# Optimization experiments

Hardware: AMD Instinct MI355X
Metric: run time of the kernel (lower is better)

## Reference

```python
import jax, jax.numpy as jnp
import numpy as np

N_NODES, N_EDGES, N_GRAPHS = 100000, 1600000, 1000
DIN, DMID, DGLOB, DOUT = 128, 128, 64, 2


def setup_inputs() -> dict:
    key = jax.random.key(0)
    ks = jax.random.split(key, 12)
    x = jax.random.normal(ks[0], (N_NODES, DIN), dtype=jnp.float32)
    edge_index = jax.random.randint(ks[1], (2, N_EDGES), 0, N_NODES, dtype=jnp.int64 if jax.config.jax_enable_x64 else jnp.int32)
    u = jax.random.normal(ks[2], (N_GRAPHS, DGLOB), dtype=jnp.float32)
    batch = jnp.sort(jax.random.randint(ks[3], (N_NODES,), 0, N_GRAPHS))
    s = 1.0 / np.sqrt(DMID)
    W1 = jax.random.normal(ks[4], (DIN, DMID), dtype=jnp.float32) * s
    b1 = jnp.zeros((DMID,), dtype=jnp.float32)
    W2 = jax.random.normal(ks[5], (DMID, DMID), dtype=jnp.float32) * s
    b2 = jnp.zeros((DMID,), dtype=jnp.float32)
    Wh1 = jax.random.normal(ks[6], (DMID + DGLOB, DMID), dtype=jnp.float32) * s
    bh1 = jnp.zeros((DMID,), dtype=jnp.float32)
    Wh2 = jax.random.normal(ks[7], (DMID, DOUT), dtype=jnp.float32) * s
    bh2 = jnp.zeros((DOUT,), dtype=jnp.float32)
    return {"x": x, "edge_index": edge_index, "u": u, "batch": batch,
            "batch_size": N_GRAPHS, "W1": W1, "b1": b1, "W2": W2, "b2": b2,
            "Wh1": Wh1, "bh1": bh1, "Wh2": Wh2, "bh2": bh2}


def _gcn_conv(x, W, b, row, col, norm, n):
    # PyG GCNConv: linear transform then symmetric-normalized scatter-add
    h = x @ W                                    # [N, dmid]
    msg = norm[:, None] * h[row]                 # gather along source nodes
    out = jax.ops.segment_sum(msg, col, num_segments=n)  # scatter to dst
    return out + b


def reference(x, edge_index, u, batch, batch_size, W1, b1, W2, b2, Wh1, bh1, Wh2, bh2):
    n = x.shape[0]
    # add self-loops (GCNConv default, edge_weight=None -> all-ones weights)
    loop = jnp.arange(n, dtype=edge_index.dtype)
    row = jnp.concatenate([edge_index[0], loop])
    col = jnp.concatenate([edge_index[1], loop])
    deg = jax.ops.segment_sum(jnp.ones_like(col, dtype=x.dtype), col, num_segments=n)
    dinv = jnp.where(deg > 0, jax.lax.rsqrt(jnp.maximum(deg, 1e-12)), 0.0)
    norm = dinv[row] * dinv[col]                 # D^-1/2 A D^-1/2, shared by both layers

    h = jax.nn.relu(_gcn_conv(x, W1, b1, row, col, norm, n))
    h = jax.nn.relu(_gcn_conv(h, W2, b2, row, col, norm, n))

    # mean pool per graph
    sums = jax.ops.segment_sum(h, batch, num_segments=batch_size)
    cnt = jax.ops.segment_sum(jnp.ones((n,), dtype=h.dtype), batch, num_segments=batch_size)
    graph_emb = sums / jnp.maximum(cnt, 1.0)[:, None]

    hcat = jnp.concatenate([graph_emb, u], axis=-1)
    # head MLP (dropout in eval mode = identity)
    out = jax.nn.relu(hcat @ Wh1 + bh1) @ Wh2 + bh2
    return out
```

## Files before the change

kernel.cpp:

```cpp
#include <hip/hip_runtime.h>
#include <hip/hip_bf16.h>

#define NN 100000
#define NE 1600000
#define NG 1000
#define NBK 196
#define BSH 9
#define SLOT 10240
#define SLOTC 12288

typedef short short8 __attribute__((ext_vector_type(8)));
typedef float f32x4 __attribute__((ext_vector_type(4)));
typedef float f32x2 __attribute__((ext_vector_type(2)));

static inline int cdiv(int a, int b) { return (a + b - 1) / b; }

__device__ __forceinline__ unsigned short f2b(float f) {
    unsigned int u = __float_as_uint(f);
    u += 0x7fff + ((u >> 16) & 1);
    return (unsigned short)(u >> 16);
}
__device__ __forceinline__ unsigned int pack2(float lo, float hi) {
    return (unsigned int)f2b(lo) | ((unsigned int)f2b(hi) << 16);
}

template <int W>
__device__ __forceinline__ f32x2 f8_2f(unsigned int v) {
    return __builtin_amdgcn_cvt_pk_f32_fp8((int)v, W);
}
__device__ __forceinline__ unsigned int f2f8_lo(float a, float b, unsigned int old) {
    return (unsigned int)__builtin_amdgcn_cvt_pk_fp8_f32(a, b, (int)old, false);
}
__device__ __forceinline__ unsigned int f2f8_hi(float a, float b, unsigned int old) {
    return (unsigned int)__builtin_amdgcn_cvt_pk_fp8_f32(a, b, (int)old, true);
}
__device__ __forceinline__ unsigned char f2f8s(float a) {
    return (unsigned char)(__builtin_amdgcn_cvt_pk_fp8_f32(a, a, 0, false) & 0xFF);
}

__global__ __launch_bounds__(256) void k_prep(const float* __restrict__ W1,
                                              const float* __restrict__ W2,
                                              const float* __restrict__ b1,
                                              const float* __restrict__ b2,
                                              unsigned short* __restrict__ Wt1,
                                              unsigned char* __restrict__ Wt2p,
                                              float* __restrict__ b1p,
                                              float* __restrict__ b2p,
                                              int* __restrict__ gcur,
                                              const int* __restrict__ batch,
                                              int* __restrict__ gstart,
                                              unsigned char* __restrict__ Hs8) {
    int b = blockIdx.x, t = threadIdx.x;
    if (b < 128) {
        if (t < 128) {
            Wt1[b * 128 + t] = f2b(W1[t * 128 + b]);
        } else {
            int q = t - 128;
            int c = (q & 7) * 16 + (q >> 3);
            Wt2p[b * 128 + q] = f2f8s(W2[c * 128 + b]);
        }
    } else if (b == 128) {
        if (t < NBK) gcur[t] = t * SLOT;
        if (t < 128) {
            int c = (t & 7) * 16 + (t >> 3);
            b1p[t] = b1[c];
            b2p[t] = b2[c];
        }
        if (t >= 128 && t < 136) {
            uint4 z; z.x = 0u; z.y = 0u; z.z = 0u; z.w = 0u;
            ((uint4*)(Hs8 + (size_t)NN * 128))[t - 128] = z;
        }
    } else {
        int n = (b - 129) * 256 + t;
        if (n <= NN) {
            int cur = (n == NN) ? NG : batch[n];
            int prev = (n == 0) ? -1 : batch[n - 1];
            for (int g = prev + 1; g <= cur; g++) gstart[g] = n;
        }
    }
}

__global__ __launch_bounds__(256) void k_bin2(const int* __restrict__ row,
                                              const int* __restrict__ col,
                                              int* __restrict__ gcur,
                                              unsigned int* __restrict__ tmp) {
    __shared__ unsigned int ent[4000];
    __shared__ unsigned int srt[4000];
    __shared__ unsigned char bkt[4000];
    __shared__ unsigned char bky[4000];
    __shared__ int cnt[NBK];
    __shared__ int gbase[NBK];
    __shared__ int lbase[NBK];
    __shared__ int sh[256];
    int t = threadIdx.x;
    if (t < NBK) cnt[t] = 0;
    __syncthreads();
    const int q0 = blockIdx.x * 1000;
    const int4* col4 = (const int4*)col;
    const int4* row4 = (const int4*)row;
#pragma unroll
    for (int it = 0; it < 4; it++) {
        int idx = it * 256 + t;
        if (idx < 1000) {
            int4 c = col4[q0 + idx];
            int4 r = row4[q0 + idx];
            int d, b;
            d = c.x; b = d >> BSH; atomicAdd(&cnt[b], 1);
            ent[idx * 4 + 0] = ((unsigned int)(d & 511) << 17) | (unsigned int)r.x;
            bkt[idx * 4 + 0] = (unsigned char)b;
            d = c.y; b = d >> BSH; atomicAdd(&cnt[b], 1);
            ent[idx * 4 + 1] = ((unsigned int)(d & 511) << 17) | (unsigned int)r.y;
            bkt[idx * 4 + 1] = (unsigned char)b;
            d = c.z; b = d >> BSH; atomicAdd(&cnt[b], 1);
            ent[idx * 4 + 2] = ((unsigned int)(d & 511) << 17) | (unsigned int)r.z;
            bkt[idx * 4 + 2] = (unsigned char)b;
            d = c.w; b = d >> BSH; atomicAdd(&cnt[b], 1);
            ent[idx * 4 + 3] = ((unsigned int)(d & 511) << 17) | (unsigned int)r.w;
            bkt[idx * 4 + 3] = (unsigned char)b;
        }
    }
    __syncthreads();
    int v = (t < NBK) ? cnt[t] : 0;
    sh[t] = v;
    __syncthreads();
    for (int d = 1; d < 256; d <<= 1) {
        int u = (t >= d) ? sh[t - d] : 0;
        __syncthreads();
        sh[t] += u;
        __syncthreads();
    }
    if (t < NBK) {
        lbase[t] = sh[t] - v;
        gbase[t] = atomicAdd(&gcur[t], v);
        cnt[t] = sh[t] - v;
    }
    __syncthreads();
#pragma unroll
    for (int it = 0; it < 16; it++) {
        int i = it * 256 + t;
        if (i < 4000) {
            int b = bkt[i];
            int p = atomicAdd(&cnt[b], 1);
            srt[p] = ent[i];
            bky[p] = (unsigned char)b;
        }
    }
    __syncthreads();
#pragma unroll
    for (int it = 0; it < 16; it++) {
        int i = it * 256 + t;
        if (i < 4000) {
            int b = bky[i];
            tmp[gbase[b] + (i - lbase[b])] = srt[i];
        }
    }
}

__global__ __launch_bounds__(1024) void k_bucket(const unsigned int* __restrict__ tmp,
                                                 const int* __restrict__ gcur,
                                                 unsigned int* __restrict__ meta,
                                                 float* __restrict__ dinv,
                                                 int* __restrict__ csr_src) {
    __shared__ int cnt[512];
    __shared__ int loff[512];
    __shared__ int send[512];
    __shared__ int sh[256];
    int b = blockIdx.x, t = threadIdx.x;
    int j0 = b << BSH;
    int nd = min(512, NN - j0);
    int rb = b * SLOT;
    int rbc = b * SLOTC;
    int m = gcur[b] - rb;
    if (t < 512) cnt[t] = 0;
    __syncthreads();
    for (int i = t; i < m; i += 1024)
        atomicAdd(&cnt[tmp[rb + i] >> 17], 1);
    __syncthreads();
    int r0 = 0, r1 = 0, p0 = 0, ts = 0;
    if (t < 256) {
        r0 = cnt[2 * t]; r1 = cnt[2 * t + 1];
        p0 = (r0 + 7) & ~7;
        int p1 = (r1 + 7) & ~7;
        ts = p0 + p1;
        sh[t] = ts;
    }
    __syncthreads();
    for (int d = 1; d < 256; d <<= 1) {
        int u = (t >= d && t < 256) ? sh[t - d] : 0;
        __syncthreads();
        if (t < 256) sh[t] += u;
        __syncthreads();
    }
    if (t < 256) {
        int ex = sh[t] - ts;
        loff[2 * t] = ex;
        loff[2 * t + 1] = ex + p0;
    }
    __syncthreads();
    for (int j = t; j < nd; j += 1024) {
        int o = rbc + loff[j];
        int dg = cnt[j];
        int dgp = (dg + 7) & ~7;
        meta[j0 + j] = (unsigned int)o | ((unsigned int)dgp << 22);
        send[j] = o + dgp;
        dinv[j0 + j] = rsqrtf((float)(dg + 1));
        cnt[j] = o;
    }
    __syncthreads();
    for (int i = t; i < m; i += 1024) {
        unsigned int e = tmp[rb + i];
        int d = e >> 17;
        int s = (int)(e & 0x1FFFFu);
        int p = atomicAdd(&cnt[d], 1);
        csr_src[p] = s;
    }
    __syncthreads();
    for (int j = t; j < nd; j += 1024) {
        int pe = send[j];
        for (int p = cnt[j]; p < pe; p++) csr_src[p] = NN;
    }
}

__global__ __launch_bounds__(256) void k_gemm1(const float* __restrict__ X,
                                               const unsigned short* __restrict__ Wt,
                                               const float* __restrict__ dinv,
                                               unsigned char* __restrict__ Hs8) {
    __shared__ __align__(16) unsigned short Ws[128 * 128];
    int t = threadIdx.x;
#pragma unroll
    for (int i = 0; i < 8; i++) {
        int id = t + i * 256;
        int n = id >> 4, c = id & 15;
        *(short8*)((char*)Ws + n * 256 + ((c ^ (n & 15)) << 4)) =
            *(const short8*)(Wt + n * 128 + c * 8);
    }
    __syncthreads();

    int lane = t & 63, wid = t >> 6;
    int n16 = lane & 15, quad = lane >> 4;
    int row_base = blockIdx.x * 128 + wid * 32;

    short8 a[2][4];
#pragma unroll
    for (int rt = 0; rt < 2; rt++) {
        int r = row_base + rt * 16 + n16;
        if (r > NN - 1) r = NN - 1;
        const float* ap = X + (size_t)r * 128 + quad * 8;
#pragma unroll
        for (int ks = 0; ks < 4; ks++) {
            float4 v0 = *(const float4*)(ap + ks * 32);
            float4 v1 = *(const float4*)(ap + ks * 32 + 4);
            uint4 up;
            up.x = pack2(v0.x, v0.y); up.y = pack2(v0.z, v0.w);
            up.z = pack2(v1.x, v1.y); up.w = pack2(v1.z, v1.w);
            a[rt][ks] = *(short8*)&up;
        }
    }

    f32x4 acc[2][8];
#pragma unroll
    for (int rt = 0; rt < 2; rt++)
#pragma unroll
        for (int ct = 0; ct < 8; ct++)
            acc[rt][ct] = (f32x4){0.f, 0.f, 0.f, 0.f};

#pragma unroll
    for (int ks = 0; ks < 4; ks++) {
#pragma unroll
        for (int ct = 0; ct < 8; ct++) {
            short8 b = *(const short8*)((const char*)Ws +
                        (ct * 16 + n16) * 256 + ((((ks << 2) + quad) ^ n16) << 4));
            acc[0][ct] = __builtin_amdgcn_mfma_f32_16x16x32_bf16(a[0][ks], b, acc[0][ct], 0, 0, 0);
            acc[1][ct] = __builtin_amdgcn_mfma_f32_16x16x32_bf16(a[1][ks], b, acc[1][ct], 0, 0, 0);
        }
    }

#pragma unroll
    for (int rt = 0; rt < 2; rt++) {
#pragma unroll
        for (int reg = 0; reg < 4; reg++) {
            int row = row_base + rt * 16 + quad * 4 + reg;
            if (row < NN) {
                float di = dinv[row];
                unsigned int u0 = 0, u1 = 0;
                u0 = f2f8_lo(acc[rt][0][reg] * di, acc[rt][1][reg] * di, u0);
                u0 = f2f8_hi(acc[rt][2][reg] * di, acc[rt][3][reg] * di, u0);
                u1 = f2f8_lo(acc[rt][4][reg] * di, acc[rt][5][reg] * di, u1);
                u1 = f2f8_hi(acc[rt][6][reg] * di, acc[rt][7][reg] * di, u1);
                uint2 o; o.x = u0; o.y = u1;
                ((uint2*)(Hs8 + (size_t)row * 128))[n16] = o;
            }
        }
    }
}

__global__ __launch_bounds__(256) void k_gemm2(const unsigned char* __restrict__ A8,
                                               const unsigned char* __restrict__ Wt2p,
                                               const float* __restrict__ dinv,
                                               unsigned char* __restrict__ Hs8) {
    __shared__ __align__(16) unsigned char Ws[128 * 128];
    int t = threadIdx.x;
#pragma unroll
    for (int i = 0; i < 8; i++) {
        int id = t + i * 256;
        int n = id >> 4, c = id & 15;
        *(uint2*)(Ws + n * 128 + ((c ^ (n & 15)) << 3)) =
            *(const uint2*)(Wt2p + n * 128 + c * 8);
    }
    __syncthreads();

    int lane = t & 63, wid = t >> 6;
    int n16 = lane & 15, quad = lane >> 4;
    int row_base = blockIdx.x * 128 + wid * 32;

    uint2 a[2][4];
#pragma unroll
    for (int rt = 0; rt < 2; rt++) {
        int r = row_base + rt * 16 + n16;
        if (r > NN - 1) r = NN - 1;
        const unsigned char* ap = A8 + (size_t)r * 128 + quad * 8;
#pragma unroll
        for (int ks = 0; ks < 4; ks++)
            a[rt][ks] = *(const uint2*)(ap + ks * 32);
    }

    f32x4 acc[2][8];
#pragma unroll
    for (int rt = 0; rt < 2; rt++)
#pragma unroll
        for (int ct = 0; ct < 8; ct++)
            acc[rt][ct] = (f32x4){0.f, 0.f, 0.f, 0.f};

#pragma unroll
    for (int ks = 0; ks < 4; ks++) {
        long a0 = __builtin_bit_cast(long, a[0][ks]);
        long a1 = __builtin_bit_cast(long, a[1][ks]);
#pragma unroll
        for (int ct = 0; ct < 8; ct++) {
            uint2 bv = *(const uint2*)(Ws + (ct * 16 + n16) * 128 +
                                       ((((ks << 2) + quad) ^ n16) << 3));
            long bb = __builtin_bit_cast(long, bv);
            acc[0][ct] = __builtin_amdgcn_mfma_f32_16x16x32_fp8_fp8(a0, bb, acc[0][ct], 0, 0, 0);
            acc[1][ct] = __builtin_amdgcn_mfma_f32_16x16x32_fp8_fp8(a1, bb, acc[1][ct], 0, 0, 0);
        }
    }

#pragma unroll
    for (int rt = 0; rt < 2; rt++) {
#pragma unroll
        for (int reg = 0; reg < 4; reg++) {
            int row = row_base + rt * 16 + quad * 4 + reg;
            if (row < NN) {
                float di = dinv[row];
                unsigned int u0 = 0, u1 = 0;
                u0 = f2f8_lo(acc[rt][0][reg] * di, acc[rt][1][reg] * di, u0);
                u0 = f2f8_hi(acc[rt][2][reg] * di, acc[rt][3][reg] * di, u0);
                u1 = f2f8_lo(acc[rt][4][reg] * di, acc[rt][5][reg] * di, u1);
                u1 = f2f8_hi(acc[rt][6][reg] * di, acc[rt][7][reg] * di, u1);
                uint2 o; o.x = u0; o.y = u1;
                ((uint2*)(Hs8 + (size_t)row * 128))[n16] = o;
            }
        }
    }
}

__global__ __launch_bounds__(256) void k_agg(const unsigned char* __restrict__ Hb,
                                             const unsigned int* __restrict__ meta,
                                             const int* __restrict__ csr_src,
                                             const float* __restrict__ dinv,
                                             const float* __restrict__ biasp,
                                             unsigned char* __restrict__ outp) {
    int node = blockIdx.x * 16 + (threadIdx.x >> 4);
    int li = threadIdx.x & 15;
    unsigned lo8 = (unsigned)li * 8u;
    unsigned int md = meta[node];
    int base = (int)(md & 0x3FFFFFu);
    int degp = (int)(md >> 22);
    f32x2 A0 = {0.f, 0.f}, A1 = {0.f, 0.f}, A2 = {0.f, 0.f}, A3 = {0.f, 0.f};
#define LDH(idx) (*(const uint2*)(Hb + (unsigned)(idx) * 128u + lo8))
#define ACC8(V) { \
        A0 += f8_2f<0>((V).x); A1 += f8_2f<1>((V).x); \
        A2 += f8_2f<0>((V).y); A3 += f8_2f<1>((V).y); }
    uint2 v = LDH(node);
    const int4* ip = (const int4*)(csr_src + base);
    int4 i0 = ip[0], i1 = ip[1], i2 = ip[2], i3 = ip[3];
    ACC8(v)
    for (int e0 = 0; e0 < degp; e0 += 16) {
        uint2 w0 = LDH(i0.x), w1 = LDH(i0.y), w2 = LDH(i0.z), w3 = LDH(i0.w);
        uint2 w4 = LDH(i1.x), w5 = LDH(i1.y), w6 = LDH(i1.z), w7 = LDH(i1.w);
        uint2 w8 = {0, 0}, w9 = {0, 0}, wA = {0, 0}, wB = {0, 0};
        uint2 wC = {0, 0}, wD = {0, 0}, wE = {0, 0}, wF = {0, 0};
        if (e0 + 8 < degp) {
            w8 = LDH(i2.x); w9 = LDH(i2.y); wA = LDH(i2.z); wB = LDH(i2.w);
            wC = LDH(i3.x); wD = LDH(i3.y); wE = LDH(i3.z); wF = LDH(i3.w);
        }
        if (e0 + 16 < degp) {
            const int4* np = (const int4*)(csr_src + base + e0 + 16);
            i0 = np[0]; i1 = np[1]; i2 = np[2]; i3 = np[3];
        }
        ACC8(w0) ACC8(w1) ACC8(w2) ACC8(w3)
        ACC8(w4) ACC8(w5) ACC8(w6) ACC8(w7)
        ACC8(w8) ACC8(w9) ACC8(wA) ACC8(wB)
        ACC8(wC) ACC8(wD) ACC8(wE) ACC8(wF)
    }
#undef ACC8
#undef LDH
    float di = dinv[node];
    const float4* b4 = (const float4*)biasp;
    float4 bA = b4[li * 2], bB = b4[li * 2 + 1];
    float r0 = fmaxf(fmaf(di, A0[0], bA.x), 0.f);
    float r1 = fmaxf(fmaf(di, A0[1], bA.y), 0.f);
    float r2 = fmaxf(fmaf(di, A1[0], bA.z), 0.f);
    float r3 = fmaxf(fmaf(di, A1[1], bA.w), 0.f);
    float r4 = fmaxf(fmaf(di, A2[0], bB.x), 0.f);
    float r5 = fmaxf(fmaf(di, A2[1], bB.y), 0.f);
    float r6 = fmaxf(fmaf(di, A3[0], bB.z), 0.f);
    float r7 = fmaxf(fmaf(di, A3[1], bB.w), 0.f);
    unsigned int u0 = 0, u1 = 0;
    u0 = f2f8_lo(r0, r1, u0); u0 = f2f8_hi(r2, r3, u0);
    u1 = f2f8_lo(r4, r5, u1); u1 = f2f8_hi(r6, r7, u1);
    uint2 o; o.x = u0; o.y = u1;
    *(uint2*)(outp + (unsigned)node * 128u + lo8) = o;
}

__global__ __launch_bounds__(256) void k_poolhead(const unsigned char* __restrict__ A,
                                                  const int* __restrict__ gstart,
                                                  const float* __restrict__ u,
                                                  const float* __restrict__ Wh1,
                                                  const float* __restrict__ bh1,
                                                  const float* __restrict__ Wh2,
                                                  const float* __restrict__ bh2,
                                                  float* __restrict__ out) {
    int g = blockIdx.x, t = threadIdx.x;
    int start = gstart[g];
    int end = gstart[g + 1];

    int li = t & 7;
    int ri = t >> 3;
    float acc[16];
#pragma unroll
    for (int j = 0; j < 16; j++) acc[j] = 0.f;
    f32x2 p;
    for (int i = start + ri; i < end; i += 32) {
        uint4 v = ((const uint4*)A)[(size_t)i * 8 + li];
#define UP(VV, base) p = f8_2f<0>(VV); acc[base] += p.x; acc[base+1] += p.y; \
                     p = f8_2f<1>(VV); acc[base+2] += p.x; acc[base+3] += p.y;
        UP(v.x, 0) UP(v.y, 4) UP(v.z, 8) UP(v.w, 12)
#undef UP
    }
#pragma unroll
    for (int j = 0; j < 16; j++) {
        acc[j] += __shfl_xor(acc[j], 8);
        acc[j] += __shfl_xor(acc[j], 16);
        acc[j] += __shfl_xor(acc[j], 32);
    }
    __shared__ float part[4][128];
    __shared__ float hc[192];
    __shared__ float tt[128];
    int w = t >> 6;
    if ((t & 63) < 8) {
#pragma unroll
        for (int j = 0; j < 16; j++) part[w][li * 16 + j] = acc[j];
    }
    __syncthreads();
    float cntf = (float)max(end - start, 1);
    if (t < 128) {
        int q = (t & 15) * 8 + (t >> 4);
        hc[t] = (part[0][q] + part[1][q] + part[2][q] + part[3][q]) / cntf;
    } else if (t < 192) {
        hc[t] = u[g * 64 + (t - 128)];
    }
    __syncthreads();
    if (t < 128) {
        float a2 = bh1[t];
        for (int k = 0; k < 192; k++) a2 = fmaf(hc[k], Wh1[k * 128 + t], a2);
        tt[t] = fmaxf(a2, 0.f);
    }
    __syncthreads();
    if (t < 2) {
        float o = bh2[t];
        for (int c2 = 0; c2 < 128; c2++) o = fmaf(tt[c2], Wh2[c2 * 2 + t], o);
        out[g * 2 + t] = o;
    }
}

extern "C" void kernel_launch(void* const* d_in, const int* in_sizes, int n_in,
                              void* d_out, int out_size, void* d_ws, size_t ws_size,
                              hipStream_t stream) {
    const float* x   = (const float*)d_in[0];
    const int*   ei  = (const int*)d_in[1];
    const int*   row = ei;
    const int*   col = ei + NE;
    const float* u   = (const float*)d_in[2];
    const int*   batch = (const int*)d_in[3];
    const float* W1  = (const float*)d_in[5];
    const float* b1  = (const float*)d_in[6];
    const float* W2  = (const float*)d_in[7];
    const float* b2  = (const float*)d_in[8];
    const float* Wh1 = (const float*)d_in[9];
    const float* bh1 = (const float*)d_in[10];
    const float* Wh2 = (const float*)d_in[11];
    const float* bh2 = (const float*)d_in[12];
    float* out = (float*)d_out;

    char* ws = (char*)d_ws;
    size_t o = 0;
    auto alloc = [&](size_t bytes) -> void* {
        void* p = ws + o;
        o += (bytes + 511) & ~(size_t)511;
        return p;
    };
    unsigned char*  Hs8 = (unsigned char*)alloc((size_t)(NN + 1) * 128);
    unsigned char*  A1b = (unsigned char*)alloc((size_t)NN * 128);
    unsigned char*  A2b = (unsigned char*)alloc((size_t)NN * 128);
    unsigned short* Wt1 = (unsigned short*)alloc((size_t)128 * 128 * 2);
    unsigned char*  Wt2p= (unsigned char*)alloc((size_t)128 * 128);
    float* b1p    = (float*)alloc((size_t)128 * 4);
    float* b2p    = (float*)alloc((size_t)128 * 4);
    float* dinv   = (float*)alloc((size_t)NN * 4);
    unsigned int* meta = (unsigned int*)alloc((size_t)NN * 4);
    int*   csr_src= (int*)alloc((size_t)NBK * SLOTC * 4 + 512);
    unsigned int* tmp = (unsigned int*)alloc((size_t)NBK * SLOT * 4);
    int*   gcur   = (int*)alloc((size_t)256 * 4);
    int*   gstart = (int*)alloc((size_t)(NG + 1) * 4);

    k_prep<<<129 + cdiv(NN + 1, 256), 256, 0, stream>>>(W1, W2, b1, b2, Wt1, Wt2p,
                                                        b1p, b2p, gcur, batch, gstart, Hs8);
    k_bin2<<<400, 256, 0, stream>>>(row, col, gcur, tmp);
    k_bucket<<<NBK, 1024, 0, stream>>>(tmp, gcur, meta, dinv, csr_src);

    k_gemm1<<<cdiv(NN, 128), 256, 0, stream>>>(x, Wt1, dinv, Hs8);
    k_agg<<<NN / 16, 256, 0, stream>>>(Hs8, meta, csr_src, dinv, b1p, A1b);
    k_gemm2<<<cdiv(NN, 128), 256, 0, stream>>>(A1b, Wt2p, dinv, Hs8);
    k_agg<<<NN / 16, 256, 0, stream>>>(Hs8, meta, csr_src, dinv, b2p, A2b);

    k_poolhead<<<NG, 256, 0, stream>>>(A2b, gstart, u, Wh1, bh1, Wh2, bh2, out);
}
```

Baseline: 238.7 us.

## Sort nodes by degree for aggregation load balancing and cache bucket entries in LDS

Builds a per-node degree histogram in k_bucket and adds scan and scatter kernels that produce a permutation of nodes in descending padded-degree order. Both aggregation launches then process nodes through this permutation, so each block holds nodes of similar degree and lanes waste less time waiting on long neighbour lists. k_bucket also keeps its edge slot in shared memory so the second pass does not re-read it from global memory, and the pooling head uses a shuffle reduction for the final 2-output layer instead of two serial threads. The cost is two extra small launches, an indirect node lookup in aggregation, scattered output writes, and loss of node locality between neighbouring blocks.

```diff
diff --git a/kernel.cpp b/kernel.cpp
--- a/kernel.cpp
+++ b/kernel.cpp
@@ -49,7 +49,8 @@
                                               int* __restrict__ gcur,
                                               const int* __restrict__ batch,
                                               int* __restrict__ gstart,
-                                              unsigned char* __restrict__ Hs8) {
+                                              unsigned char* __restrict__ Hs8,
+                                              int* __restrict__ dbins) {
     int b = blockIdx.x, t = threadIdx.x;
     if (b < 128) {
         if (t < 128) {
@@ -70,6 +71,7 @@
             uint4 z; z.x = 0u; z.y = 0u; z.z = 0u; z.w = 0u;
             ((uint4*)(Hs8 + (size_t)NN * 128))[t - 128] = z;
         }
+        if (t >= 192) dbins[t - 192] = 0;
     } else {
         int n = (b - 129) * 256 + t;
         if (n <= NN) {
@@ -160,11 +162,14 @@
                                                  const int* __restrict__ gcur,
                                                  unsigned int* __restrict__ meta,
                                                  float* __restrict__ dinv,
-                                                 int* __restrict__ csr_src) {
+                                                 int* __restrict__ csr_src,
+                                                 int* __restrict__ dbins) {
+    __shared__ unsigned int sent[SLOT];
     __shared__ int cnt[512];
     __shared__ int loff[512];
     __shared__ int send[512];
     __shared__ int sh[256];
+    __shared__ int lbin[64];
     int b = blockIdx.x, t = threadIdx.x;
     int j0 = b << BSH;
     int nd = min(512, NN - j0);
@@ -172,9 +177,13 @@
     int rbc = b * SLOTC;
     int m = gcur[b] - rb;
     if (t < 512) cnt[t] = 0;
-    __syncthreads();
-    for (int i = t; i < m; i += 1024)
-        atomicAdd(&cnt[tmp[rb + i] >> 17], 1);
+    if (t < 64) lbin[t] = 0;
+    __syncthreads();
+    for (int i = t; i < m; i += 1024) {
+        unsigned int e = tmp[rb + i];
+        sent[i] = e;
+        atomicAdd(&cnt[e >> 17], 1);
+    }
     __syncthreads();
     int r0 = 0, r1 = 0, p0 = 0, ts = 0;
     if (t < 256) {
@@ -204,11 +213,12 @@
         meta[j0 + j] = (unsigned int)o | ((unsigned int)dgp << 22);
         send[j] = o + dgp;
         dinv[j0 + j] = rsqrtf((float)(dg + 1));
+        atomicAdd(&lbin[63 - min(dgp >> 3, 63)], 1);
         cnt[j] = o;
     }
     __syncthreads();
     for (int i = t; i < m; i += 1024) {
-        unsigned int e = tmp[rb + i];
+        unsigned int e = sent[i];
         int d = e >> 17;
         int s = (int)(e & 0x1FFFFu);
         int p = atomicAdd(&cnt[d], 1);
@@ -219,6 +229,36 @@
         int pe = send[j];
         for (int p = cnt[j]; p < pe; p++) csr_src[p] = NN;
     }
+    if (t < 64 && lbin[t]) atomicAdd(&dbins[t], lbin[t]);
+}
+
+__global__ void k_scan(const int* __restrict__ dbins, int* __restrict__ gbincur) {
+    if (threadIdx.x == 0) {
+        int s = 0;
+        for (int i = 0; i < 64; i++) { gbincur[i] = s; s += dbins[i]; }
+    }
+}
+
+__global__ __launch_bounds__(256) void k_scatter(const unsigned int* __restrict__ meta,
+                                                 int* __restrict__ gbincur,
+                                                 int* __restrict__ perm) {
+    __shared__ int lcnt[64];
+    __shared__ int lbase[64];
+    int t = threadIdx.x;
+    int node = blockIdx.x * 256 + t;
+    if (t < 64) lcnt[t] = 0;
+    __syncthreads();
+    int bin = 0, rank = 0;
+    bool ok = node < NN;
+    if (ok) {
+        int dgp = (int)(meta[node] >> 22);
+        bin = 63 - min(dgp >> 3, 63);
+        rank = atomicAdd(&lcnt[bin], 1);
+    }
+    __syncthreads();
+    if (t < 64 && lcnt[t] > 0) lbase[t] = atomicAdd(&gbincur[t], lcnt[t]);
+    __syncthreads();
+    if (ok) perm[lbase[bin] + rank] = node;
 }
 
 __global__ __launch_bounds__(256) void k_gemm1(const float* __restrict__ X,
@@ -369,8 +409,9 @@
                                              const int* __restrict__ csr_src,
                                              const float* __restrict__ dinv,
                                              const float* __restrict__ biasp,
+                                             const int* __restrict__ perm,
                                              unsigned char* __restrict__ outp) {
-    int node = blockIdx.x * 16 + (threadIdx.x >> 4);
+    int node = perm[blockIdx.x * 16 + (threadIdx.x >> 4)];
     int li = threadIdx.x & 15;
     unsigned lo8 = (unsigned)li * 8u;
     unsigned int md = meta[node];
@@ -457,6 +498,7 @@
     __shared__ float part[4][128];
     __shared__ float hc[192];
     __shared__ float tt[128];
+    __shared__ float red[8];
     int w = t >> 6;
     if ((t & 63) < 8) {
 #pragma unroll
@@ -473,15 +515,26 @@
     __syncthreads();
     if (t < 128) {
         float a2 = bh1[t];
+#pragma unroll 8
         for (int k = 0; k < 192; k++) a2 = fmaf(hc[k], Wh1[k * 128 + t], a2);
         tt[t] = fmaxf(a2, 0.f);
     }
     __syncthreads();
-    if (t < 2) {
-        float o = bh2[t];
-        for (int c2 = 0; c2 < 128; c2++) o = fmaf(tt[c2], Wh2[c2 * 2 + t], o);
-        out[g * 2 + t] = o;
-    }
+    float p0 = 0.f, p1 = 0.f;
+    if (t < 128) {
+        float vv = tt[t];
+        p0 = vv * Wh2[t * 2];
+        p1 = vv * Wh2[t * 2 + 1];
+    }
+#pragma unroll
+    for (int d = 32; d >= 1; d >>= 1) {
+        p0 += __shfl_xor(p0, d);
+        p1 += __shfl_xor(p1, d);
+    }
+    if ((t & 63) == 0) { red[w * 2] = p0; red[w * 2 + 1] = p1; }
+    __syncthreads();
+    if (t == 0) out[g * 2 + 0] = bh2[0] + red[0] + red[2];
+    if (t == 1) out[g * 2 + 1] = bh2[1] + red[1] + red[3];
 }
 
 extern "C" void kernel_launch(void* const* d_in, const int* in_sizes, int n_in,
@@ -523,16 +576,22 @@
     unsigned int* tmp = (unsigned int*)alloc((size_t)NBK * SLOT * 4);
     int*   gcur   = (int*)alloc((size_t)256 * 4);
     int*   gstart = (int*)alloc((size_t)(NG + 1) * 4);
+    int*   dbins  = (int*)alloc((size_t)64 * 4);
+    int*   gbincur= (int*)alloc((size_t)64 * 4);
+    int*   perm   = (int*)alloc((size_t)NN * 4);
 
     k_prep<<<129 + cdiv(NN + 1, 256), 256, 0, stream>>>(W1, W2, b1, b2, Wt1, Wt2p,
-                                                        b1p, b2p, gcur, batch, gstart, Hs8);
+                                                        b1p, b2p, gcur, batch, gstart,
+                                                        Hs8, dbins);
     k_bin2<<<400, 256, 0, stream>>>(row, col, gcur, tmp);
-    k_bucket<<<NBK, 1024, 0, stream>>>(tmp, gcur, meta, dinv, csr_src);
+    k_bucket<<<NBK, 1024, 0, stream>>>(tmp, gcur, meta, dinv, csr_src, dbins);
+    k_scan<<<1, 64, 0, stream>>>(dbins, gbincur);
+    k_scatter<<<cdiv(NN, 256), 256, 0, stream>>>(meta, gbincur, perm);
 
     k_gemm1<<<cdiv(NN, 128), 256, 0, stream>>>(x, Wt1, dinv, Hs8);
-    k_agg<<<NN / 16, 256, 0, stream>>>(Hs8, meta, csr_src, dinv, b1p, A1b);
+    k_agg<<<NN / 16, 256, 0, stream>>>(Hs8, meta, csr_src, dinv, b1p, perm, A1b);
     k_gemm2<<<cdiv(NN, 128), 256, 0, stream>>>(A1b, Wt2p, dinv, Hs8);
-    k_agg<<<NN / 16, 256, 0, stream>>>(Hs8, meta, csr_src, dinv, b2p, A2b);
+    k_agg<<<NN / 16, 256, 0, stream>>>(Hs8, meta, csr_src, dinv, b2p, perm, A2b);
 
     k_poolhead<<<NG, 256, 0, stream>>>(A2b, gstart, u, Wh1, bh1, Wh2, bh2, out);
 }
```

Result: slower. 245.8 us (+3.0%).

## Fuse layer-2 GEMM into first aggregation kernel and cache bucket entries in LDS

Applied to the files above, without the earlier changes.

The standalone second GEMM is folded into the first aggregation kernel. Each 16-node block stages its aggregated fp8 rows in shared memory and one wave runs the 128x128 fp8 MFMA, writing the dinv-scaled result directly. This removes a kernel launch and the round trip of the intermediate activation through global memory, but every aggregation block now reloads the 16 KB weight tile into LDS and only one wave does the matmul. The bucket kernel also keeps its edge entries in LDS to avoid a second global read, and the head's final dot product becomes a shuffle reduction.

```diff
diff --git a/kernel.cpp b/kernel.cpp
--- a/kernel.cpp
+++ b/kernel.cpp
@@ -49,7 +49,8 @@
                                               int* __restrict__ gcur,
                                               const int* __restrict__ batch,
                                               int* __restrict__ gstart,
-                                              unsigned char* __restrict__ Hs8) {
+                                              unsigned char* __restrict__ Hs8,
+                                              unsigned char* __restrict__ Hg2) {
     int b = blockIdx.x, t = threadIdx.x;
     if (b < 128) {
         if (t < 128) {
@@ -69,6 +70,10 @@
         if (t >= 128 && t < 136) {
             uint4 z; z.x = 0u; z.y = 0u; z.z = 0u; z.w = 0u;
             ((uint4*)(Hs8 + (size_t)NN * 128))[t - 128] = z;
+        }
+        if (t >= 136 && t < 144) {
+            uint4 z; z.x = 0u; z.y = 0u; z.z = 0u; z.w = 0u;
+            ((uint4*)(Hg2 + (size_t)NN * 128))[t - 136] = z;
         }
     } else {
         int n = (b - 129) * 256 + t;
@@ -161,6 +166,7 @@
                                                  unsigned int* __restrict__ meta,
                                                  float* __restrict__ dinv,
                                                  int* __restrict__ csr_src) {
+    __shared__ unsigned int sent[SLOT];
     __shared__ int cnt[512];
     __shared__ int loff[512];
     __shared__ int send[512];
@@ -173,8 +179,11 @@
     int m = gcur[b] - rb;
     if (t < 512) cnt[t] = 0;
     __syncthreads();
-    for (int i = t; i < m; i += 1024)
-        atomicAdd(&cnt[tmp[rb + i] >> 17], 1);
+    for (int i = t; i < m; i += 1024) {
+        unsigned int e = tmp[rb + i];
+        sent[i] = e;
+        atomicAdd(&cnt[e >> 17], 1);
+    }
     __syncthreads();
     int r0 = 0, r1 = 0, p0 = 0, ts = 0;
     if (t < 256) {
@@ -208,7 +217,7 @@
     }
     __syncthreads();
     for (int i = t; i < m; i += 1024) {
-        unsigned int e = tmp[rb + i];
+        unsigned int e = sent[i];
         int d = e >> 17;
         int s = (int)(e & 0x1FFFFu);
         int p = atomicAdd(&cnt[d], 1);
@@ -294,84 +303,28 @@
     }
 }
 
-__global__ __launch_bounds__(256) void k_gemm2(const unsigned char* __restrict__ A8,
-                                               const unsigned char* __restrict__ Wt2p,
-                                               const float* __restrict__ dinv,
-                                               unsigned char* __restrict__ Hs8) {
-    __shared__ __align__(16) unsigned char Ws[128 * 128];
-    int t = threadIdx.x;
-#pragma unroll
-    for (int i = 0; i < 8; i++) {
-        int id = t + i * 256;
-        int n = id >> 4, c = id & 15;
-        *(uint2*)(Ws + n * 128 + ((c ^ (n & 15)) << 3)) =
-            *(const uint2*)(Wt2p + n * 128 + c * 8);
-    }
-    __syncthreads();
-
-    int lane = t & 63, wid = t >> 6;
-    int n16 = lane & 15, quad = lane >> 4;
-    int row_base = blockIdx.x * 128 + wid * 32;
-
-    uint2 a[2][4];
-#pragma unroll
-    for (int rt = 0; rt < 2; rt++) {
-        int r = row_base + rt * 16 + n16;
-        if (r > NN - 1) r = NN - 1;
-        const unsigned char* ap = A8 + (size_t)r * 128 + quad * 8;
-#pragma unroll
-        for (int ks = 0; ks < 4; ks++)
-            a[rt][ks] = *(const uint2*)(ap + ks * 32);
-    }
-
-    f32x4 acc[2][8];
-#pragma unroll
-    for (int rt = 0; rt < 2; rt++)
-#pragma unroll
-        for (int ct = 0; ct < 8; ct++)
-            acc[rt][ct] = (f32x4){0.f, 0.f, 0.f, 0.f};
-
-#pragma unroll
-    for (int ks = 0; ks < 4; ks++) {
-        long a0 = __builtin_bit_cast(long, a[0][ks]);
-        long a1 = __builtin_bit_cast(long, a[1][ks]);
-#pragma unroll
-        for (int ct = 0; ct < 8; ct++) {
-            uint2 bv = *(const uint2*)(Ws + (ct * 16 + n16) * 128 +
-                                       ((((ks << 2) + quad) ^ n16) << 3));
-            long bb = __builtin_bit_cast(long, bv);
-            acc[0][ct] = __builtin_amdgcn_mfma_f32_16x16x32_fp8_fp8(a0, bb, acc[0][ct], 0, 0, 0);
-            acc[1][ct] = __builtin_amdgcn_mfma_f32_16x16x32_fp8_fp8(a1, bb, acc[1][ct], 0, 0, 0);
-        }
-    }
-
-#pragma unroll
-    for (int rt = 0; rt < 2; rt++) {
-#pragma unroll
-        for (int reg = 0; reg < 4; reg++) {
-            int row = row_base + rt * 16 + quad * 4 + reg;
-            if (row < NN) {
-                float di = dinv[row];
-                unsigned int u0 = 0, u1 = 0;
-                u0 = f2f8_lo(acc[rt][0][reg] * di, acc[rt][1][reg] * di, u0);
-                u0 = f2f8_hi(acc[rt][2][reg] * di, acc[rt][3][reg] * di, u0);
-                u1 = f2f8_lo(acc[rt][4][reg] * di, acc[rt][5][reg] * di, u1);
-                u1 = f2f8_hi(acc[rt][6][reg] * di, acc[rt][7][reg] * di, u1);
-                uint2 o; o.x = u0; o.y = u1;
-                ((uint2*)(Hs8 + (size_t)row * 128))[n16] = o;
-            }
-        }
-    }
-}
-
+template <int FUSE>
 __global__ __launch_bounds__(256) void k_agg(const unsigned char* __restrict__ Hb,
                                              const unsigned int* __restrict__ meta,
                                              const int* __restrict__ csr_src,
                                              const float* __restrict__ dinv,
                                              const float* __restrict__ biasp,
+                                             const unsigned char* __restrict__ Wt2p,
                                              unsigned char* __restrict__ outp) {
-    int node = blockIdx.x * 16 + (threadIdx.x >> 4);
-    int li = threadIdx.x & 15;
+    __shared__ __align__(16) unsigned char sm[FUSE ? (128 * 128 + 16 * 128) : 16];
+    int t = threadIdx.x;
+    if (FUSE) {
+#pragma unroll
+        for (int i = 0; i < 8; i++) {
+            int id = t + i * 256;
+            int n = id >> 4, c = id & 15;
+            *(uint2*)(sm + n * 128 + ((c ^ (n & 15)) << 3)) =
+                *(const uint2*)(Wt2p + n * 128 + c * 8);
+        }
+    }
+    int sub = t >> 4;
+    int node = blockIdx.x * 16 + sub;
+    int li = t & 15;
     unsigned lo8 = (unsigned)li * 8u;
     unsigned int md = meta[node];
     int base = (int)(md & 0x3FFFFFu);
@@ -420,7 +373,43 @@
     u0 = f2f8_lo(r0, r1, u0); u0 = f2f8_hi(r2, r3, u0);
     u1 = f2f8_lo(r4, r5, u1); u1 = f2f8_hi(r6, r7, u1);
     uint2 o; o.x = u0; o.y = u1;
-    *(uint2*)(outp + (unsigned)node * 128u + lo8) = o;
+    if (!FUSE) {
+        *(uint2*)(outp + (unsigned)node * 128u + lo8) = o;
+        return;
+    }
+    *(uint2*)(sm + 16384 + sub * 128 + (((li ^ sub) & 15) << 3)) = o;
+    __syncthreads();
+    if (t < 64) {
+        int n16 = t & 15, quad = t >> 4;
+        f32x4 acc[8];
+#pragma unroll
+        for (int ct = 0; ct < 8; ct++) acc[ct] = (f32x4){0.f, 0.f, 0.f, 0.f};
+#pragma unroll
+        for (int ks = 0; ks < 4; ks++) {
+            uint2 av = *(const uint2*)(sm + 16384 + n16 * 128 +
+                                       ((((ks << 2) + quad) ^ n16) << 3));
+            long aa = __builtin_bit_cast(long, av);
+#pragma unroll
+            for (int ct = 0; ct < 8; ct++) {
+                uint2 bv = *(const uint2*)(sm + (ct * 16 + n16) * 128 +
+                                           ((((ks << 2) + quad) ^ n16) << 3));
+                long bb = __builtin_bit_cast(long, bv);
+                acc[ct] = __builtin_amdgcn_mfma_f32_16x16x32_fp8_fp8(aa, bb, acc[ct], 0, 0, 0);
+            }
+        }
+#pragma unroll
+        for (int reg = 0; reg < 4; reg++) {
+            int row = blockIdx.x * 16 + quad * 4 + reg;
+            float d2 = dinv[row];
+            unsigned int g0 = 0, g1 = 0;
+            g0 = f2f8_lo(acc[0][reg] * d2, acc[1][reg] * d2, g0);
+            g0 = f2f8_hi(acc[2][reg] * d2, acc[3][reg] * d2, g0);
+            g1 = f2f8_lo(acc[4][reg] * d2, acc[5][reg] * d2, g1);
+            g1 = f2f8_hi(acc[6][reg] * d2, acc[7][reg] * d2, g1);
+            uint2 go; go.x = g0; go.y = g1;
+            ((uint2*)(outp + (size_t)row * 128))[n16] = go;
+        }
+    }
 }
 
 __global__ __launch_bounds__(256) void k_poolhead(const unsigned char* __restrict__ A,
@@ -457,6 +446,7 @@
     __shared__ float part[4][128];
     __shared__ float hc[192];
     __shared__ float tt[128];
+    __shared__ float red[8];
     int w = t >> 6;
     if ((t & 63) < 8) {
 #pragma unroll
@@ -473,15 +463,26 @@
     __syncthreads();
     if (t < 128) {
         float a2 = bh1[t];
+#pragma unroll 8
         for (int k = 0; k < 192; k++) a2 = fmaf(hc[k], Wh1[k * 128 + t], a2);
         tt[t] = fmaxf(a2, 0.f);
     }
     __syncthreads();
-    if (t < 2) {
-        float o = bh2[t];
-        for (int c2 = 0; c2 < 128; c2++) o = fmaf(tt[c2], Wh2[c2 * 2 + t], o);
-        out[g * 2 + t] = o;
-    }
+    float p0 = 0.f, p1 = 0.f;
+    if (t < 128) {
+        float vv = tt[t];
+        p0 = vv * Wh2[t * 2];
+        p1 = vv * Wh2[t * 2 + 1];
+    }
+#pragma unroll
+    for (int d = 32; d >= 1; d >>= 1) {
+        p0 += __shfl_xor(p0, d);
+        p1 += __shfl_xor(p1, d);
+    }
+    if ((t & 63) == 0) { red[w * 2] = p0; red[w * 2 + 1] = p1; }
+    __syncthreads();
+    if (t == 0) out[g * 2 + 0] = bh2[0] + red[0] + red[2];
+    if (t == 1) out[g * 2 + 1] = bh2[1] + red[1] + red[3];
 }
 
 extern "C" void kernel_launch(void* const* d_in, const int* in_sizes, int n_in,
@@ -511,7 +512,7 @@
         return p;
     };
     unsigned char*  Hs8 = (unsigned char*)alloc((size_t)(NN + 1) * 128);
-    unsigned char*  A1b = (unsigned char*)alloc((size_t)NN * 128);
+    unsigned char*  Hg2 = (unsigned char*)alloc((size_t)(NN + 1) * 128);
     unsigned char*  A2b = (unsigned char*)alloc((size_t)NN * 128);
     unsigned short* Wt1 = (unsigned short*)alloc((size_t)128 * 128 * 2);
     unsigned char*  Wt2p= (unsigned char*)alloc((size_t)128 * 128);
@@ -525,14 +526,14 @@
     int*   gstart = (int*)alloc((size_t)(NG + 1) * 4);
 
     k_prep<<<129 + cdiv(NN + 1, 256), 256, 0, stream>>>(W1, W2, b1, b2, Wt1, Wt2p,
-                                                        b1p, b2p, gcur, batch, gstart, Hs8);
+                                                        b1p, b2p, gcur, batch, gstart,
+                                                        Hs8, Hg2);
     k_bin2<<<400, 256, 0, stream>>>(row, col, gcur, tmp);
     k_bucket<<<NBK, 1024, 0, stream>>>(tmp, gcur, meta, dinv, csr_src);
 
     k_gemm1<<<cdiv(NN, 128), 256, 0, stream>>>(x, Wt1, dinv, Hs8);
-    k_agg<<<NN / 16, 256, 0, stream>>>(Hs8, meta, csr_src, dinv, b1p, A1b);
-    k_gemm2<<<cdiv(NN, 128), 256, 0, stream>>>(A1b, Wt2p, dinv, Hs8);
-    k_agg<<<NN / 16, 256, 0, stream>>>(Hs8, meta, csr_src, dinv, b2p, A2b);
+    k_agg<1><<<NN / 16, 256, 0, stream>>>(Hs8, meta, csr_src, dinv, b1p, Wt2p, Hg2);
+    k_agg<0><<<NN / 16, 256, 0, stream>>>(Hg2, meta, csr_src, dinv, b2p, nullptr, A2b);
 
     k_poolhead<<<NG, 256, 0, stream>>>(A2b, gstart, u, Wh1, bh1, Wh2, bh2, out);
 }
```

New measurement: 232.6 us. 2.6% less time.
